# Kernel optimization log

Hardware: AMD Instinct MI355X
Metric: run time of the kernel (lower is better)

## Reference

```python
import jax, jax.numpy as jnp
import numpy as np

N, H = 16, 200
EMB, H1, H2 = 64, 128, 64
NUM_SKILLS = 2000
D_USER, D_ITEM, D_LANG = 100, 100, 10
TIME_BINS = np.array([1, 3600, 24 * 3600, 7 * 24 * 3600], dtype=np.float32)
NUM_TIME_CATS = TIME_BINS.size + 2  # 6

# strictly-lower-triangular pair indices, row-major: pair (i, j) with j < i
PAIR_I, PAIR_J = np.tril_indices(H, k=-1)          # skill_indices, history_indices_selected
P = PAIR_I.size                                    # adjusted_history_len = H*(H-1)/2
ar = np.arange(H)
SUM_IDX = np.concatenate([ar * (ar - 1) // 2, [H * (H - 1) // 2]]).astype(np.int64)  # len H+1


def setup_inputs() -> dict:
    key = jax.random.key(0)
    ks = jax.random.split(key, 16)
    users = jax.random.normal(ks[0], (N, D_USER), jnp.float32)
    items = jax.random.normal(ks[1], (N * H, D_ITEM), jnp.float32)
    langs = jax.random.normal(ks[2], (N * H, D_LANG), jnp.float32)
    skills = jax.random.randint(ks[3], (N, H), 0, NUM_SKILLS)
    timestamps = jnp.sort(jax.random.uniform(ks[4], (N, H), jnp.float32) * 2e6, axis=1)
    targets = (jax.random.uniform(ks[5], (N, H)) > 0.5).astype(jnp.float32)
    mask = jnp.ones((N * H,), dtype=bool)
    emb_table = jax.random.normal(ks[6], (NUM_SKILLS, EMB), jnp.float32) * 0.1
    emb_table = emb_table.at[0].set(0.0)  # padding_idx=0
    W1 = jax.random.normal(ks[7], (H1, 2 * EMB + NUM_TIME_CATS), jnp.float32) * 0.05
    b1 = jnp.zeros((H1,), jnp.float32)
    W2 = jax.random.normal(ks[8], (H2, H1), jnp.float32) * 0.05
    b2 = jnp.zeros((H2,), jnp.float32)
    W3 = jax.random.normal(ks[9], (1, H2), jnp.float32) * 0.05
    b3 = jnp.zeros((1,), jnp.float32)
    num_features = D_USER + D_ITEM + D_LANG + NUM_SKILLS
    linW = jax.random.normal(ks[10], (1, num_features + 2 * NUM_SKILLS), jnp.float32) * 0.01
    linb = jnp.zeros((1,), jnp.float32)
    return {"users": users, "items": items, "langs": langs, "skills": skills,
            "timestamps": timestamps, "targets": targets, "mask": mask,
            "emb_table": emb_table, "W1": W1, "b1": b1, "W2": W2, "b2": b2,
            "W3": W3, "b3": b3, "linW": linW, "linb": linb}


def _forward(users, items, langs, skills, timestamps, targets, mask,
             emb_table, W1, b1, W2, b2, W3, b3, linW, linb):
    bins = jnp.asarray(TIME_BINS)
    pi = jnp.asarray(PAIR_I)
    pj = jnp.asarray(PAIR_J)
    # gather pair embeddings: [N*P, EMB]
    emb = emb_table[skills]                       # [N, H, EMB]
    e_i = emb[:, pi].reshape(-1, EMB)             # skill at position i
    e_j = emb[:, pj].reshape(-1, EMB)             # history skill j < i
    # time-delta categories
    dt = (timestamps[:, pi] - timestamps[:, pj]).reshape(-1)
    cats = jnp.sum(dt[:, None] > bins[None, :], axis=1) + 1
    pad = skills == 0
    pad_pair = pad[:, pi].reshape(-1) | pad[:, pj].reshape(-1)
    cats = jnp.where(pad_pair, 0, cats)
    dt_oh = jax.nn.one_hot(cats, NUM_TIME_CATS, dtype=jnp.float32)
    # pairwise similarity MLP -> tanh scalar, [N, P]
    x = jnp.concatenate([e_i, e_j, dt_oh], axis=1)
    h = jax.nn.relu(x @ W1.T + b1)
    h = jax.nn.relu(h @ W2.T + b2)
    sim = jnp.tanh(h @ W3.T + b3).reshape(N, P)

    sum_idx = jnp.asarray(SUM_IDX)

    def seg_sum(v):  # cumsum-based segment sum over pairs grouped by i -> [N, H]
        cs = jnp.concatenate([jnp.zeros((N, 1), v.dtype), jnp.cumsum(v, axis=1)], axis=1)
        return cs[:, sum_idx[1:]] - cs[:, sum_idx[:-1]]

    flat_skills = skills.reshape(-1)              # [N*H]
    padf = (flat_skills != 0).astype(jnp.float32)
    rows = jnp.arange(N * H)
    v_total = seg_sum(sim).reshape(-1) * padf
    v_correct = seg_sum(sim * targets[:, pi]).reshape(-1) * padf
    tcf = jnp.zeros((N * H, 2 * NUM_SKILLS), jnp.float32)
    tcf = tcf.at[rows, flat_skills].set(v_total)
    tcf = tcf.at[rows, flat_skills + NUM_SKILLS].set(v_correct)

    feats = jnp.concatenate([
        jnp.repeat(users, H, axis=0), items, langs,
        jax.nn.one_hot(flat_skills, NUM_SKILLS, dtype=jnp.float32), tcf], axis=1)
    logits = feats @ linW.T + linb                # [N*H, 1]
    preds = logits.reshape(-1)
    labels = targets.reshape(-1)
    maskf = mask.astype(jnp.float32)
    # BCEWithLogits (reduction='none') + z-term, z_weight=0.0; mask applied as weight
    bce = jnp.logaddexp(0.0, preds) - preds * labels
    eps = 1e-6
    yc = jnp.clip(labels, eps, 1.0 - eps)
    z = jnp.log(yc / (1.0 - yc))
    z_weight = 0.0
    loss = (bce + z_weight * jnp.square(z - preds)) * maskf
    return loss, jax.nn.sigmoid(preds), labels


def reference(users, items, langs, skills, timestamps, targets, mask,
              emb_table, W1, b1, W2, b2, W3, b3, linW, linb):
    return _forward(users, items, langs, skills, timestamps, targets, mask,
                    emb_table, W1, b1, W2, b2, W3, b3, linW, linb)
```

## Files before the change

### kernel.cpp

```cpp
#include <hip/hip_runtime.h>
#include <math.h>

#define N_B     16
#define H_LEN   200
#define NH      3200
#define EMB     64
#define HID1    128
#define HID2    64
#define NCAT    6
#define W1_COLS 134

#define TI 16
#define NTILE_I 13
#define NTRI (NTILE_I * (NTILE_I + 1) / 2)

#define WS_VT   0
#define WS_W2F  3200
#define WS_W1F  7296
#define WS_CF   15488
#define WS_A    16256
#define WS_B    425856

typedef __attribute__((ext_vector_type(8))) __bf16 bf16x8;
typedef __attribute__((ext_vector_type(8))) unsigned short ushort8;
typedef __attribute__((ext_vector_type(4))) float f32x4;

__device__ __forceinline__ unsigned short bfbits(float x) {
    return __builtin_bit_cast(unsigned short, (__bf16)x);
}

__global__ void k0_setup(const float* __restrict__ W1,
                         const float* __restrict__ b1,
                         const float* __restrict__ W2,
                         float* __restrict__ ws) {
    int idx = blockIdx.x * 256 + threadIdx.x;
    if (idx < 16384) {
        int e = idx & 7, l = (idx >> 3) & 63, ks = (idx >> 9) & 1;
        int nt = (idx >> 10) & 7, h = idx >> 13;
        int col = l & 15, quad = l >> 4;
        int c = nt * 16 + col;
        int kg = h * EMB + ks * 32 + quad * 8 + e;
        ((unsigned short*)(ws + WS_W1F))[idx] = bfbits(W1[c * W1_COLS + kg]);
        return;
    }
    idx -= 16384;
    if (idx < 8192) {
        int e = idx & 7, lane = (idx >> 3) & 63, f = idx >> 9;
        int mt = f >> 2, kk = f & 3, col = lane & 15, quad = lane >> 4;
        float w = W2[(mt * 16 + col) * HID1 + (kk * 4 + quad) * 8 + e];
        ((unsigned short*)(ws + WS_W2F))[idx] = bfbits(w);
        return;
    }
    idx -= 8192;
    if (idx < NCAT * HID1) {
        int c = idx >> 7, t = idx & 127;
        ws[WS_CF + idx] = W1[t * W1_COLS + 2 * EMB + c] + b1[t];
        return;
    }
    idx -= NCAT * HID1;
    if (idx < NH) ws[WS_VT + idx] = 0.f;
}

__global__ __launch_bounds__(256)
void k1_mfma(const int* __restrict__ skills,
             const float* __restrict__ emb,
             float* __restrict__ ws) {
    __shared__ float esm[32][68];
    int t = threadIdx.x, lane = t & 63, w = t >> 6;
    int col = lane & 15, quad = lane >> 4;
    int r0 = blockIdx.x * 32;

    #pragma unroll
    for (int it = 0; it < 2; ++it) {
        int f = t + it * 256;
        int r = f >> 4, c4 = f & 15;
        int s = skills[r0 + r];
        *(f32x4*)&esm[r][c4 * 4] = *(const f32x4*)(emb + (size_t)s * EMB + c4 * 4);
    }
    __syncthreads();

    int h = w & 1;
    int rbase = (w >> 1) * 16;
    const ushort8* w1f = (const ushort8*)(ws + WS_W1F) + h * 16 * 64;
    f32x4 acc[8] = {{0,0,0,0},{0,0,0,0},{0,0,0,0},{0,0,0,0},
                    {0,0,0,0},{0,0,0,0},{0,0,0,0},{0,0,0,0}};
    #pragma unroll
    for (int ks = 0; ks < 2; ++ks) {
        f32x4 a0 = *(const f32x4*)&esm[rbase + col][ks * 32 + quad * 8];
        f32x4 a1 = *(const f32x4*)&esm[rbase + col][ks * 32 + quad * 8 + 4];
        bf16x8 af;
        #pragma unroll
        for (int e = 0; e < 4; ++e) { af[e] = (__bf16)a0[e]; af[4 + e] = (__bf16)a1[e]; }
        #pragma unroll
        for (int nt = 0; nt < 8; ++nt) {
            bf16x8 bf = __builtin_bit_cast(bf16x8, w1f[(nt * 2 + ks) * 64 + lane]);
            acc[nt] = __builtin_amdgcn_mfma_f32_16x16x32_bf16(af, bf, acc[nt], 0, 0, 0);
        }
    }
    float* dst = ws + (h ? WS_B : WS_A);
    #pragma unroll
    for (int nt = 0; nt < 8; ++nt)
        #pragma unroll
        for (int r = 0; r < 4; ++r)
            dst[(size_t)(r0 + rbase + quad * 4 + r) * HID1 + nt * 16 + col] = acc[nt][r];
}

__global__ __launch_bounds__(256, 2)
void k2_mfma(const int* __restrict__ skills,
             const float* __restrict__ ts,
             const float* __restrict__ b2,
             const float* __restrict__ W3,
             const float* __restrict__ b3,
             float* __restrict__ ws) {
    __shared__ float Asm[TI][132];
    __shared__ float Bsm[TI][132];
    __shared__ float Csm[NCAT][132];
    __shared__ float tsi[TI], tsj[TI];
    __shared__ int   ski[TI], skj[TI];

    int t = threadIdx.x, lane = t & 63, w = t >> 6;
    int col = lane & 15, quad = lane >> 4;

    int bid = blockIdx.x;
    int n = bid & 15;
    int tt = bid >> 4;
    int ti = (int)((sqrtf(8.f * (float)tt + 1.f) - 1.f) * 0.5f);
    while (ti * (ti + 1) / 2 > tt) --ti;
    while ((ti + 1) * (ti + 2) / 2 <= tt) ++ti;
    int tj = tt - ti * (ti + 1) / 2;
    int i0 = ti * TI, j0 = tj * TI;
    int base = n * H_LEN;
    bool diag = (ti == tj);

    const ushort8* w2f = (const ushort8*)(ws + WS_W2F);
    bf16x8 afr[4][4];
    #pragma unroll
    for (int mt = 0; mt < 4; ++mt)
        #pragma unroll
        for (int kk = 0; kk < 4; ++kk)
            afr[mt][kk] = __builtin_bit_cast(bf16x8, w2f[(mt * 4 + kk) * 64 + lane]);
    float b2v[16], w3v[16];
    #pragma unroll
    for (int mt = 0; mt < 4; ++mt)
        #pragma unroll
        for (int r = 0; r < 4; ++r) {
            int u = mt * 16 + quad * 4 + r;
            b2v[mt * 4 + r] = b2[u];
            w3v[mt * 4 + r] = W3[u];
        }
    float b3s = b3[0];

    {
        #pragma unroll
        for (int it = 0; it < 2; ++it) {
            int f = t + it * 256;
            int r = f >> 5, c4 = f & 31;
            int gi = min(i0 + r, H_LEN - 1);
            int gj = min(j0 + r, H_LEN - 1);
            *(f32x4*)&Asm[r][c4 * 4] = *(const f32x4*)(ws + WS_A + (size_t)(base + gi) * HID1 + c4 * 4);
            *(f32x4*)&Bsm[r][c4 * 4] = *(const f32x4*)(ws + WS_B + (size_t)(base + gj) * HID1 + c4 * 4);
        }
        if (t < NCAT * 32) {
            int cr = t >> 5, cc = t & 31;
            *(f32x4*)&Csm[cr][cc * 4] = *(const f32x4*)(ws + WS_CF + cr * HID1 + cc * 4);
        }
        if (t < TI) {
            int gii = min(i0 + t, H_LEN - 1);
            int gjj = min(j0 + t, H_LEN - 1);
            tsi[t] = ts[base + gii]; ski[t] = skills[base + gii];
            tsj[t] = ts[base + gjj]; skj[t] = skills[base + gjj];
        }
    }
    __syncthreads();

    f32x4 braw[8];
    #pragma unroll
    for (int kk = 0; kk < 4; ++kk) {
        braw[2 * kk]     = *(const f32x4*)&Bsm[col][kk * 32 + quad * 8];
        braw[2 * kk + 1] = *(const f32x4*)&Bsm[col][kk * 32 + quad * 8 + 4];
    }
    int sj = skj[col]; float tsjv = tsj[col];

    #pragma unroll
    for (int s = 0; s < 4; ++s) {
        int ii = w * 4 + s;
        int gi = i0 + ii;
        if (gi >= H_LEN) continue;
        if (diag && ii == 0) continue;

        int si = ski[ii];  float tsiv = tsi[ii];
        float dtv = tsiv - tsjv;
        int cat = (si == 0 || sj == 0) ? 0
                : 1 + (dtv > 1.f) + (dtv > 3600.f) + (dtv > 86400.f) + (dtv > 604800.f);

        f32x4 acc[4];
        #pragma unroll
        for (int mt = 0; mt < 4; ++mt) {
            acc[mt][0] = b2v[mt * 4 + 0]; acc[mt][1] = b2v[mt * 4 + 1];
            acc[mt][2] = b2v[mt * 4 + 2]; acc[mt][3] = b2v[mt * 4 + 3];
        }
        #pragma unroll
        for (int kk = 0; kk < 4; ++kk) {
            f32x4 a0 = *(const f32x4*)&Asm[ii][kk * 32 + quad * 8];
            f32x4 a1 = *(const f32x4*)&Asm[ii][kk * 32 + quad * 8 + 4];
            f32x4 c0 = *(const f32x4*)&Csm[cat][kk * 32 + quad * 8];
            f32x4 c1 = *(const f32x4*)&Csm[cat][kk * 32 + quad * 8 + 4];
            f32x4 t0 = a0 + braw[2 * kk] + c0;
            f32x4 t1 = a1 + braw[2 * kk + 1] + c1;
            t0 = __builtin_elementwise_max(t0, (f32x4)0.f);
            t1 = __builtin_elementwise_max(t1, (f32x4)0.f);
            bf16x8 v;
            #pragma unroll
            for (int e = 0; e < 4; ++e) { v[e] = (__bf16)t0[e]; v[4 + e] = (__bf16)t1[e]; }
            #pragma unroll
            for (int mt = 0; mt < 4; ++mt)
                acc[mt] = __builtin_amdgcn_mfma_f32_16x16x32_bf16(
                    afr[mt][kk], v, acc[mt], 0, 0, 0);
        }

        float partial = 0.f;
        #pragma unroll
        for (int mt = 0; mt < 4; ++mt)
            #pragma unroll
            for (int r = 0; r < 4; ++r) {
                float h2 = fmaxf(acc[mt][r], 0.f);
                partial = fmaf(h2, w3v[mt * 4 + r], partial);
            }
        partial += __shfl_xor(partial, 16);
        partial += __shfl_xor(partial, 32);
        float xc = fminf(fmaxf(partial + b3s, -15.f), 15.f);
        float e2 = __expf(2.f * xc);
        float sim = (e2 - 1.f) / (e2 + 1.f);

        int gj = j0 + col;
        bool valid = (gj < gi);
        sim = valid ? sim : 0.f;
        sim += __shfl_xor(sim, 1);
        sim += __shfl_xor(sim, 2);
        sim += __shfl_xor(sim, 4);
        sim += __shfl_xor(sim, 8);
        if (lane == 0) atomicAdd(&ws[WS_VT + base + gi], sim);
    }
}

__global__ __launch_bounds__(256)
void k3_final(const float* __restrict__ users,
              const float* __restrict__ items,
              const float* __restrict__ langs,
              const int* __restrict__ skills,
              const float* __restrict__ targets,
              const float* __restrict__ linW,
              const float* __restrict__ linb,
              const float* __restrict__ ws,
              float* __restrict__ out) {
    int r = blockIdx.x * 4 + (threadIdx.x >> 6);
    int lane = threadIdx.x & 63;
    int n = r / H_LEN;
    float acc = 0.f;
    for (int idx = lane; idx < 210; idx += 64) {
        float f;
        if (idx < 100)      f = users[n * 100 + idx];
        else if (idx < 200) f = items[r * 100 + (idx - 100)];
        else                f = langs[r * 10 + (idx - 200)];
        acc = fmaf(f, linW[idx], acc);
    }
    #pragma unroll
    for (int off = 32; off > 0; off >>= 1) acc += __shfl_xor(acc, off);
    if (lane == 0) {
        int s = skills[r];
        float tgt = targets[r];
        float vtv = ws[WS_VT + r];
        if (s == 0) vtv = 0.f;
        float vcv = vtv * tgt;
        float logit = acc + linW[210 + s] + vtv * linW[2210 + s]
                    + vcv * linW[4210 + s] + linb[0];
        float sp = logit > 0.f ? logit + log1pf(expf(-logit)) : log1pf(expf(logit));
        float loss = sp - logit * tgt;
        float sig = 1.f / (1.f + expf(-logit));
        out[r]          = loss;
        out[NH + r]     = sig;
        out[2 * NH + r] = tgt;
    }
}

extern "C" void kernel_launch(void* const* d_in, const int* in_sizes, int n_in,
                              void* d_out, int out_size, void* d_ws, size_t ws_size,
                              hipStream_t stream) {
    const float* users   = (const float*)d_in[0];
    const float* items   = (const float*)d_in[1];
    const float* langs   = (const float*)d_in[2];
    const int*   skills  = (const int*)d_in[3];
    const float* ts      = (const float*)d_in[4];
    const float* targets = (const float*)d_in[5];
    const float* emb     = (const float*)d_in[7];
    const float* W1      = (const float*)d_in[8];
    const float* b1      = (const float*)d_in[9];
    const float* W2      = (const float*)d_in[10];
    const float* b2      = (const float*)d_in[11];
    const float* W3      = (const float*)d_in[12];
    const float* b3      = (const float*)d_in[13];
    const float* linW    = (const float*)d_in[14];
    const float* linb    = (const float*)d_in[15];
    float* ws  = (float*)d_ws;
    float* out = (float*)d_out;

    hipLaunchKernelGGL(k0_setup, dim3(112), dim3(256), 0, stream, W1, b1, W2, ws);
    hipLaunchKernelGGL(k1_mfma, dim3(NH / 32), dim3(256), 0, stream, skills, emb, ws);
    hipLaunchKernelGGL(k2_mfma, dim3(N_B * NTRI), dim3(256), 0, stream,
                       skills, ts, b2, W3, b3, ws);
    hipLaunchKernelGGL(k3_final, dim3(NH / 4), dim3(256), 0, stream,
                       users, items, langs, skills, targets, linW, linb, ws, out);
}
```

Before: 111.6 us.

## Fuse first-layer embedding projection into pairwise kernel, drop separate k1 launch

Removes the k1 kernel that projected skill embeddings through W1 into global A/B buffers. Each k2 block now gathers the 16 i-row and 16 j-row embeddings itself and computes their W1 projections with MFMA into shared memory. The goal is to save one launch and the global write and read of the A/B intermediates. The cost is redundant projection work, since each row is recomputed by every tile pair that uses it, plus an extra barrier. It also folds the b2 bias into the first MFMA accumulator and vectorises the W3 dot product.

Measured after the change: 111.2 us. About the same (-0.4%).

```diff
diff --git a/kernel.cpp b/kernel.cpp
--- a/kernel.cpp
+++ b/kernel.cpp
@@ -18,8 +18,6 @@
 #define WS_W2F  3200
 #define WS_W1F  7296
 #define WS_CF   15488
-#define WS_A    16256
-#define WS_B    425856
 
 typedef __attribute__((ext_vector_type(8))) __bf16 bf16x8;
 typedef __attribute__((ext_vector_type(8))) unsigned short ushort8;
@@ -61,57 +59,16 @@
     if (idx < NH) ws[WS_VT + idx] = 0.f;
 }
 
-__global__ __launch_bounds__(256)
-void k1_mfma(const int* __restrict__ skills,
-             const float* __restrict__ emb,
-             float* __restrict__ ws) {
-    __shared__ float esm[32][68];
-    int t = threadIdx.x, lane = t & 63, w = t >> 6;
-    int col = lane & 15, quad = lane >> 4;
-    int r0 = blockIdx.x * 32;
-
-    #pragma unroll
-    for (int it = 0; it < 2; ++it) {
-        int f = t + it * 256;
-        int r = f >> 4, c4 = f & 15;
-        int s = skills[r0 + r];
-        *(f32x4*)&esm[r][c4 * 4] = *(const f32x4*)(emb + (size_t)s * EMB + c4 * 4);
-    }
-    __syncthreads();
-
-    int h = w & 1;
-    int rbase = (w >> 1) * 16;
-    const ushort8* w1f = (const ushort8*)(ws + WS_W1F) + h * 16 * 64;
-    f32x4 acc[8] = {{0,0,0,0},{0,0,0,0},{0,0,0,0},{0,0,0,0},
-                    {0,0,0,0},{0,0,0,0},{0,0,0,0},{0,0,0,0}};
-    #pragma unroll
-    for (int ks = 0; ks < 2; ++ks) {
-        f32x4 a0 = *(const f32x4*)&esm[rbase + col][ks * 32 + quad * 8];
-        f32x4 a1 = *(const f32x4*)&esm[rbase + col][ks * 32 + quad * 8 + 4];
-        bf16x8 af;
-        #pragma unroll
-        for (int e = 0; e < 4; ++e) { af[e] = (__bf16)a0[e]; af[4 + e] = (__bf16)a1[e]; }
-        #pragma unroll
-        for (int nt = 0; nt < 8; ++nt) {
-            bf16x8 bf = __builtin_bit_cast(bf16x8, w1f[(nt * 2 + ks) * 64 + lane]);
-            acc[nt] = __builtin_amdgcn_mfma_f32_16x16x32_bf16(af, bf, acc[nt], 0, 0, 0);
-        }
-    }
-    float* dst = ws + (h ? WS_B : WS_A);
-    #pragma unroll
-    for (int nt = 0; nt < 8; ++nt)
-        #pragma unroll
-        for (int r = 0; r < 4; ++r)
-            dst[(size_t)(r0 + rbase + quad * 4 + r) * HID1 + nt * 16 + col] = acc[nt][r];
-}
-
 __global__ __launch_bounds__(256, 2)
 void k2_mfma(const int* __restrict__ skills,
              const float* __restrict__ ts,
+             const float* __restrict__ emb,
              const float* __restrict__ b2,
              const float* __restrict__ W3,
              const float* __restrict__ b3,
              float* __restrict__ ws) {
+    __shared__ float esmI[TI][68];
+    __shared__ float esmJ[TI][68];
     __shared__ float Asm[TI][132];
     __shared__ float Bsm[TI][132];
     __shared__ float Csm[NCAT][132];
@@ -132,34 +89,13 @@
     int base = n * H_LEN;
     bool diag = (ti == tj);
 
-    const ushort8* w2f = (const ushort8*)(ws + WS_W2F);
-    bf16x8 afr[4][4];
-    #pragma unroll
-    for (int mt = 0; mt < 4; ++mt)
-        #pragma unroll
-        for (int kk = 0; kk < 4; ++kk)
-            afr[mt][kk] = __builtin_bit_cast(bf16x8, w2f[(mt * 4 + kk) * 64 + lane]);
-    float b2v[16], w3v[16];
-    #pragma unroll
-    for (int mt = 0; mt < 4; ++mt)
-        #pragma unroll
-        for (int r = 0; r < 4; ++r) {
-            int u = mt * 16 + quad * 4 + r;
-            b2v[mt * 4 + r] = b2[u];
-            w3v[mt * 4 + r] = W3[u];
-        }
-    float b3s = b3[0];
-
     {
-        #pragma unroll
-        for (int it = 0; it < 2; ++it) {
-            int f = t + it * 256;
-            int r = f >> 5, c4 = f & 31;
-            int gi = min(i0 + r, H_LEN - 1);
-            int gj = min(j0 + r, H_LEN - 1);
-            *(f32x4*)&Asm[r][c4 * 4] = *(const f32x4*)(ws + WS_A + (size_t)(base + gi) * HID1 + c4 * 4);
-            *(f32x4*)&Bsm[r][c4 * 4] = *(const f32x4*)(ws + WS_B + (size_t)(base + gj) * HID1 + c4 * 4);
-        }
+        int r = t >> 4, c4 = t & 15;
+        int gi = min(i0 + r, H_LEN - 1);
+        int gj = min(j0 + r, H_LEN - 1);
+        int si = skills[base + gi], sj2 = skills[base + gj];
+        *(f32x4*)&esmI[r][c4 * 4] = *(const f32x4*)(emb + (size_t)si * EMB + c4 * 4);
+        *(f32x4*)&esmJ[r][c4 * 4] = *(const f32x4*)(emb + (size_t)sj2 * EMB + c4 * 4);
         if (t < NCAT * 32) {
             int cr = t >> 5, cc = t & 31;
             *(f32x4*)&Csm[cr][cc * 4] = *(const f32x4*)(ws + WS_CF + cr * HID1 + cc * 4);
@@ -173,6 +109,53 @@
     }
     __syncthreads();
 
+    {
+        int half = w >> 1;
+        int ntb = (w & 1) * 4;
+        const ushort8* w1f = (const ushort8*)(ws + WS_W1F) + half * 1024;
+        float (*es)[68] = half ? esmJ : esmI;
+        float (*zs)[132] = half ? Bsm : Asm;
+        f32x4 acc[4] = {{0,0,0,0},{0,0,0,0},{0,0,0,0},{0,0,0,0}};
+        #pragma unroll
+        for (int ks = 0; ks < 2; ++ks) {
+            f32x4 a0 = *(const f32x4*)&es[col][ks * 32 + quad * 8];
+            f32x4 a1 = *(const f32x4*)&es[col][ks * 32 + quad * 8 + 4];
+            bf16x8 af;
+            #pragma unroll
+            for (int e = 0; e < 4; ++e) { af[e] = (__bf16)a0[e]; af[4 + e] = (__bf16)a1[e]; }
+            #pragma unroll
+            for (int ntl = 0; ntl < 4; ++ntl) {
+                bf16x8 bf = __builtin_bit_cast(bf16x8,
+                    w1f[((ntb + ntl) * 2 + ks) * 64 + lane]);
+                acc[ntl] = __builtin_amdgcn_mfma_f32_16x16x32_bf16(af, bf, acc[ntl], 0, 0, 0);
+            }
+        }
+        #pragma unroll
+        for (int ntl = 0; ntl < 4; ++ntl)
+            #pragma unroll
+            for (int r = 0; r < 4; ++r)
+                zs[quad * 4 + r][(ntb + ntl) * 16 + col] = acc[ntl][r];
+    }
+
+    const ushort8* w2f = (const ushort8*)(ws + WS_W2F);
+    bf16x8 afr[4][4];
+    #pragma unroll
+    for (int mt = 0; mt < 4; ++mt)
+        #pragma unroll
+        for (int kk = 0; kk < 4; ++kk)
+            afr[mt][kk] = __builtin_bit_cast(bf16x8, w2f[(mt * 4 + kk) * 64 + lane]);
+    f32x4 b2acc[4], w3f[4];
+    #pragma unroll
+    for (int mt = 0; mt < 4; ++mt)
+        #pragma unroll
+        for (int r = 0; r < 4; ++r) {
+            int u = mt * 16 + quad * 4 + r;
+            b2acc[mt][r] = b2[u];
+            w3f[mt][r]   = W3[u];
+        }
+    float b3s = b3[0];
+    __syncthreads();
+
     f32x4 braw[8];
     #pragma unroll
     for (int kk = 0; kk < 4; ++kk) {
@@ -194,11 +177,6 @@
                 : 1 + (dtv > 1.f) + (dtv > 3600.f) + (dtv > 86400.f) + (dtv > 604800.f);
 
         f32x4 acc[4];
-        #pragma unroll
-        for (int mt = 0; mt < 4; ++mt) {
-            acc[mt][0] = b2v[mt * 4 + 0]; acc[mt][1] = b2v[mt * 4 + 1];
-            acc[mt][2] = b2v[mt * 4 + 2]; acc[mt][3] = b2v[mt * 4 + 3];
-        }
         #pragma unroll
         for (int kk = 0; kk < 4; ++kk) {
             f32x4 a0 = *(const f32x4*)&Asm[ii][kk * 32 + quad * 8];
@@ -215,17 +193,16 @@
             #pragma unroll
             for (int mt = 0; mt < 4; ++mt)
                 acc[mt] = __builtin_amdgcn_mfma_f32_16x16x32_bf16(
-                    afr[mt][kk], v, acc[mt], 0, 0, 0);
-        }
-
-        float partial = 0.f;
-        #pragma unroll
-        for (int mt = 0; mt < 4; ++mt)
-            #pragma unroll
-            for (int r = 0; r < 4; ++r) {
-                float h2 = fmaxf(acc[mt][r], 0.f);
-                partial = fmaf(h2, w3v[mt * 4 + r], partial);
-            }
+                    afr[mt][kk], v, kk == 0 ? b2acc[mt] : acc[mt], 0, 0, 0);
+        }
+
+        f32x4 ps = {0.f, 0.f, 0.f, 0.f};
+        #pragma unroll
+        for (int mt = 0; mt < 4; ++mt) {
+            f32x4 hp = __builtin_elementwise_max(acc[mt], (f32x4)0.f);
+            ps = hp * w3f[mt] + ps;
+        }
+        float partial = (ps[0] + ps[1]) + (ps[2] + ps[3]);
         partial += __shfl_xor(partial, 16);
         partial += __shfl_xor(partial, 32);
         float xc = fminf(fmaxf(partial + b3s, -15.f), 15.f);
@@ -305,9 +282,8 @@
     float* out = (float*)d_out;
 
     hipLaunchKernelGGL(k0_setup, dim3(112), dim3(256), 0, stream, W1, b1, W2, ws);
-    hipLaunchKernelGGL(k1_mfma, dim3(NH / 32), dim3(256), 0, stream, skills, emb, ws);
     hipLaunchKernelGGL(k2_mfma, dim3(N_B * NTRI), dim3(256), 0, stream,
-                       skills, ts, b2, W3, b3, ws);
+                       skills, ts, emb, b2, W3, b3, ws);
     hipLaunchKernelGGL(k3_final, dim3(NH / 4), dim3(256), 0, stream,
                        users, items, langs, skills, targets, linW, linb, ws, out);
 }
```
